# Performance work log

Hardware: AMD Instinct MI355X
Metric: run time of the kernel (lower is better)

Reference implementation:

```python
import jax, jax.numpy as jnp
import numpy as np

B, C, H, W = 4, 128, 128, 128
K = 9          # 3x3 kernel taps
TAU, BETA = 0.5, 10.0


def conv3x3(x, w, b):
    # x: (B,Cin,H,W), w: (Cout,Cin,3,3), stride 1, padding 1
    y = jax.lax.conv_general_dilated(
        x, w, window_strides=(1, 1), padding=((1, 1), (1, 1)),
        dimension_numbers=('NCHW', 'OIHW', 'NCHW'))
    return y + b[None, :, None, None]


def bilinear_sample(x, py, px):
    # x: (B,C,H,W); py,px: (B,K,H,W) fractional coords -> (B,C,K,H,W), zero outside
    Hi, Wi = x.shape[2], x.shape[3]
    y0 = jnp.floor(py); x0 = jnp.floor(px)
    y1 = y0 + 1.0;      x1 = x0 + 1.0
    ly = py - y0; lx = px - x0
    hy = 1.0 - ly; hx = 1.0 - lx
    xf = x.reshape(x.shape[0], x.shape[1], -1)  # (B,C,HW)

    def corner(yc, xc, wgt):
        valid = (yc >= 0) & (yc <= Hi - 1) & (xc >= 0) & (xc <= Wi - 1)
        yi = jnp.clip(yc, 0, Hi - 1).astype(jnp.int32)
        xi = jnp.clip(xc, 0, Wi - 1).astype(jnp.int32)
        idx = (yi * Wi + xi).reshape(yc.shape[0], -1)  # (B, K*H*W)
        g = jax.vmap(lambda f, i: f[:, i])(xf, idx)    # (B,C,K*H*W)
        g = g.reshape(x.shape[0], x.shape[1], *yc.shape[1:])  # (B,C,K,H,W)
        return g * (wgt * valid.astype(wgt.dtype))[:, None]

    return (corner(y0, x0, hy * hx) + corner(y0, x1, hy * lx)
            + corner(y1, x0, ly * hx) + corner(y1, x1, ly * lx))


def modulated_dcn(x, offset, mask, w, b):
    # offset: (B,2K,H,W) layout (dy,dx) per tap; mask: (B,K,H,W)
    Bn, Cn, Hn, Wn = x.shape
    off = offset.reshape(Bn, K, 2, Hn, Wn)
    dy, dx = off[:, :, 0], off[:, :, 1]
    ky, kx = jnp.meshgrid(jnp.arange(3), jnp.arange(3), indexing='ij')
    base_y = (ky.reshape(-1) - 1).astype(x.dtype)  # dilation=1, padding=1, stride=1
    base_x = (kx.reshape(-1) - 1).astype(x.dtype)
    hh = jnp.arange(Hn, dtype=x.dtype)
    ww = jnp.arange(Wn, dtype=x.dtype)
    py = hh[None, None, :, None] + base_y[None, :, None, None] + dy  # (B,K,H,W)
    px = ww[None, None, None, :] + base_x[None, :, None, None] + dx
    samp = bilinear_sample(x, py, px) * mask[:, None]  # (B,C,K,H,W)
    out = jnp.einsum('bckhw,ock->bohw', samp, w.reshape(w.shape[0], w.shape[1], K))
    return out + b[None, :, None, None]


def setup_inputs() -> dict:
    key = jax.random.key(0)
    ks = jax.random.split(key, 8)
    x = jax.random.normal(ks[0], (B, C, H, W), dtype=jnp.float32)
    U = jax.random.uniform(ks[1], (B, 1, H, W), dtype=jnp.float32)
    # conv_offset_mask: (3*K, C+1, 3, 3); small scale -> offsets of O(1) pixel
    w_om = jax.random.normal(ks[2], (3 * K, C + 1, 3, 3), dtype=jnp.float32) * 0.01
    b_om = jnp.zeros((3 * K,), dtype=jnp.float32)
    kaiming = float(np.sqrt(2.0 / (C * 9)))
    w_dcn = jax.random.normal(ks[3], (C, C, 3, 3), dtype=jnp.float32) * kaiming
    b_dcn = jnp.zeros((C,), dtype=jnp.float32)
    w1 = jax.random.normal(ks[4], (C, C, 3, 3), dtype=jnp.float32) * kaiming
    b1 = jnp.zeros((C,), dtype=jnp.float32)
    w2 = jax.random.normal(ks[5], (C, C, 3, 3), dtype=jnp.float32) * float(np.sqrt(1.0 / (C * 9)))
    b2 = jnp.zeros((C,), dtype=jnp.float32)
    return {"x": x, "U": U, "w_om": w_om, "b_om": b_om, "w_dcn": w_dcn,
            "b_dcn": b_dcn, "w1": w1, "b1": b1, "w2": w2, "b2": b2}


def reference(x, U, w_om, b_om, w_dcn, b_dcn, w1, b1, w2, b2):
    U = jnp.clip(U, 0.0, 1.0)
    guide = jnp.concatenate([x, U], axis=1)                # (B,C+1,H,W)
    om = conv3x3(guide, w_om, b_om)                        # (B,3K,H,W)
    offset = om[:, :2 * K]
    mask = 2.0 * jax.nn.sigmoid(om[:, 2 * K:])
    z = modulated_dcn(x, offset, mask, w_dcn, b_dcn)
    r = jax.nn.relu(conv3x3(z, w1, b1))
    r = conv3x3(r, w2, b2)
    gate = jax.nn.sigmoid(BETA * (U - TAU))
    return jax.nn.relu(x + r * gate)
```

## Files before the change

kernel.cpp:

```cpp
#include <hip/hip_runtime.h>
#include <math.h>

typedef unsigned int uint;
typedef unsigned short ushort;
typedef __attribute__((ext_vector_type(8))) __bf16 bf16x8;
typedef __attribute__((ext_vector_type(4))) float f32x4;

#define HW 16384

__device__ __forceinline__ ushort f2bf(float f) {
    uint u = __float_as_uint(f);
    u += 0x7fffu + ((u >> 16) & 1u);
    return (ushort)(u >> 16);
}
__device__ __forceinline__ void bhmap(int& b, int& h) {
    int lin = blockIdx.y * (int)gridDim.x + blockIdx.x;
    int n = (lin & 7) * 64 + (lin >> 3);
    h = n & 127;
    b = n >> 7;
}
__device__ __forceinline__ void bhmap2(int& b, int& h, int& px0) {
    int lin = blockIdx.x;
    int n = ((lin & 7) << 7) | (lin >> 3);
    b = n >> 8;
    int rm = n & 255;
    h = rm >> 1;
    px0 = (rm & 1) << 6;
}
__device__ __forceinline__ int swz(int row, int chunk) {
    return row * 128 + ((chunk ^ (row & 15)) << 3);
}
__device__ __forceinline__ uint blend2(uint a, uint b, uint c, uint d,
                                       float w00, float w01, float w10, float w11) {
    float lo = w00 * __uint_as_float(a << 16) + w01 * __uint_as_float(b << 16)
             + w10 * __uint_as_float(c << 16) + w11 * __uint_as_float(d << 16);
    float hi = w00 * __uint_as_float(a & 0xffff0000u) + w01 * __uint_as_float(b & 0xffff0000u)
             + w10 * __uint_as_float(c & 0xffff0000u) + w11 * __uint_as_float(d & 0xffff0000u);
    uint ul = __float_as_uint(lo); ul += 0x7fffu + ((ul >> 16) & 1u);
    uint uh = __float_as_uint(hi); uh += 0x7fffu + ((uh >> 16) & 1u);
    return (ul >> 16) | ((uh >> 16) << 16);
}

__global__ __launch_bounds__(256) void prep_w(
    const float* __restrict__ wd, const float* __restrict__ w1,
    const float* __restrict__ w2, const float* __restrict__ wom,
    ushort* __restrict__ wdt, ushort* __restrict__ w1B,
    ushort* __restrict__ w2B, ushort* __restrict__ womB,
    float* __restrict__ womu)
{
    int i = blockIdx.x * 256 + threadIdx.x;
    if (i < 147456) {
        int k = i >> 14, oc = (i >> 7) & 127, ci = i & 127;
        int s = (oc * 128 + ci) * 9 + k;
        wdt[i] = f2bf(wd[s]);
        int chunk = ci >> 3, kk = chunk >> 2, quad = chunk & 3, e = ci & 7;
        int d = ((((k * 8 + (oc >> 4)) * 4 + kk) * 4 + quad) * 16 + (oc & 15)) * 8 + e;
        w1B[d] = f2bf(w1[s]);
        w2B[d] = f2bf(w2[s]);
    }
    if (i < 36864) {
        int k = i >> 12, oc = (i >> 7) & 31, ci = i & 127;
        int chunk = ci >> 3, kk = chunk >> 2, quad = chunk & 3, e = ci & 7;
        int d = ((((k * 2 + (oc >> 4)) * 4 + kk) * 4 + quad) * 16 + (oc & 15)) * 8 + e;
        womB[d] = (oc < 27) ? f2bf(wom[(oc * 129 + ci) * 9 + k]) : (ushort)0;
    }
    if (i < 288) {
        int k = i >> 5, oc = i & 31;
        womu[i] = (oc < 27) ? wom[(oc * 129 + 128) * 9 + k] : 0.f;
    }
}

__global__ __launch_bounds__(256) void prep_xt(
    const float* __restrict__ x, ushort* __restrict__ xt)
{
    int b, h; bhmap(b, h);
    const int tid = threadIdx.x;
    __shared__ __align__(16) ushort T[128 * 136];
    const int w0 = tid & 127, cg = tid >> 7;
#pragma unroll 4
    for (int it = 0; it < 64; it++) {
        int c = it * 2 + cg;
        float f = x[((size_t)(b * 128 + c)) * HW + h * 128 + w0];
        T[w0 * 136 + c] = f2bf(f);
    }
    __syncthreads();
    const int w1 = tid >> 1, half = tid & 1;
    uint4* dst = (uint4*)(xt + (((size_t)b * HW) + h * 128 + w1) * 128 + half * 64);
    const uint4* src = (const uint4*)&T[w1 * 136 + half * 64];
#pragma unroll
    for (int c8 = 0; c8 < 8; c8++) dst[c8] = src[c8];
}

__device__ __forceinline__ void stage_halo(
    ushort* Hs, const ushort* __restrict__ src, int b, int h, int px0, int tid, int nthr)
{
    for (int s = tid; s < 396; s += nthr) {
        int r = s >> 1, half = s & 1;
        int ky = r / 66, xi = r - ky * 66;
        int gy = h - 1 + ky, gx = px0 - 1 + xi;
        if ((unsigned)gy < 128u && (unsigned)gx < 128u) {
            const uint4* p = (const uint4*)(src + (((size_t)b * HW) + gy * 128 + gx) * 128 + half * 64);
#pragma unroll
            for (int c = 0; c < 8; c++) *(uint4*)&Hs[swz(r, half * 8 + c)] = p[c];
        } else {
            uint4 zz = {0, 0, 0, 0};
#pragma unroll
            for (int c = 0; c < 8; c++) *(uint4*)&Hs[swz(r, half * 8 + c)] = zz;
        }
    }
}

__global__ __launch_bounds__(256, 3) void k_om(
    const ushort* __restrict__ xt, const float* __restrict__ U,
    const ushort* __restrict__ womB, const float* __restrict__ womu,
    const float* __restrict__ bom, float* __restrict__ omt)
{
    int b, h, px0; bhmap2(b, h, px0);
    const int tid = threadIdx.x;
    const int wid = tid >> 6, lane = tid & 63, lq = lane & 15, quad = lane >> 4;

    __shared__ __align__(16) ushort Hs[198 * 128];
    __shared__ float U3[3 * 66];
    __shared__ float wu[288];

    stage_halo(Hs, xt, b, h, px0, tid, 256);
    for (int s = tid; s < 198; s += 256) {
        int ky = s / 66, xi = s - ky * 66;
        int gy = h - 1 + ky, gx = px0 - 1 + xi;
        float v = 0.f;
        if ((unsigned)gy < 128u && (unsigned)gx < 128u) {
            v = U[(size_t)b * HW + gy * 128 + gx];
            v = fminf(fmaxf(v, 0.f), 1.f);
        }
        U3[s] = v;
    }
    for (int s = tid; s < 288; s += 256) wu[s] = womu[s];

    f32x4 acc[2];
#pragma unroll
    for (int j = 0; j < 2; j++)
#pragma unroll
        for (int r = 0; r < 4; r++) acc[j][r] = 0.f;

    bf16x8 bcur[2][4], bnext[2][4];
#pragma unroll
    for (int j = 0; j < 2; j++)
#pragma unroll
        for (int kk = 0; kk < 4; kk++)
            bcur[j][kk] = *(const bf16x8*)(womB + (size_t)((j * 4 + kk) * 512) + lane * 8);

    __syncthreads();

#pragma unroll
    for (int t9 = 0; t9 < 9; t9++) {
        if (t9 < 8) {
#pragma unroll
            for (int j = 0; j < 2; j++)
#pragma unroll
                for (int kk = 0; kk < 4; kk++)
                    bnext[j][kk] = *(const bf16x8*)(womB + (size_t)((((t9 + 1) * 2 + j) * 4 + kk) * 512) + lane * 8);
        }
        const int base = (t9 / 3) * 66 + (t9 % 3) + wid * 16;
#pragma unroll
        for (int kk = 0; kk < 4; kk++) {
            int chunk = kk * 4 + quad;
            bf16x8 av = *(const bf16x8*)&Hs[swz(base + lq, chunk)];
#pragma unroll
            for (int j = 0; j < 2; j++)
                acc[j] = __builtin_amdgcn_mfma_f32_16x16x32_bf16(av, bcur[j][kk], acc[j], 0, 0, 0);
        }
#pragma unroll
        for (int j = 0; j < 2; j++)
#pragma unroll
            for (int kk = 0; kk < 4; kk++) bcur[j][kk] = bnext[j][kk];
    }

#pragma unroll
    for (int j = 0; j < 2; j++) {
        int oc = j * 16 + lq;
        if (oc < 27) {
            float bias = bom[oc];
#pragma unroll
            for (int r = 0; r < 4; r++) {
                int pix = wid * 16 + quad * 4 + r;
                float v = acc[j][r] + bias;
#pragma unroll
                for (int t = 0; t < 9; t++)
                    v += U3[(t / 3) * 66 + pix + (t % 3)] * wu[t * 32 + oc];
                if (oc >= 18) v = 2.f / (1.f + __expf(-v));
                omt[((size_t)b * HW + h * 128 + px0 + pix) * 32 + oc] = v;
            }
        }
    }
}

__global__ __launch_bounds__(512, 4) void k_dcn(
    const ushort* __restrict__ xt, const float* __restrict__ omt,
    const ushort* __restrict__ wdt, const float* __restrict__ bdcn,
    ushort* __restrict__ zt)
{
    int b, h; bhmap(b, h);
    const int tid = threadIdx.x;
    const int wid = tid >> 6, lane = tid & 63, lq = lane & 15, quad = lane >> 4;
    const int pixbase = (wid & 1) * 64, ocbase = (wid >> 1) * 32;

    __shared__ __align__(16) ushort As[128 * 128];
    __shared__ __align__(16) ushort Bs[128 * 128];
    __shared__ __align__(16) int tbl[2][128][8];

    const int sc = lane & 15;
    const int sp = lane >> 4;

    f32x4 acc[4][2];
#pragma unroll
    for (int i = 0; i < 4; i++)
#pragma unroll
        for (int j = 0; j < 2; j++)
#pragma unroll
            for (int r = 0; r < 4; r++) acc[i][j][r] = 0.f;

    const float* omrow = omt + ((size_t)b * HW + h * 128) * 32;
    const ushort* xtb = xt + (size_t)b * HW * 128;

    auto build = [&](int k, int buf) {
        if (tid < 128) {
            int p = tid;
            float dyv = omrow[p * 32 + 2 * k];
            float dxv = omrow[p * 32 + 2 * k + 1];
            float m   = omrow[p * 32 + 18 + k];
            float fy = (float)(h + k / 3 - 1) + dyv;
            float fx = (float)(p + k % 3 - 1) + dxv;
            float y0f = floorf(fy), x0f = floorf(fx);
            float ly = fy - y0f, lx = fx - x0f;
            float hy = 1.f - ly, hx = 1.f - lx;
            bool vy0 = (y0f >= 0.f) && (y0f <= 127.f);
            bool vy1 = (y0f >= -1.f) && (y0f <= 126.f);
            bool vx0 = (x0f >= 0.f) && (x0f <= 127.f);
            bool vx1 = (x0f >= -1.f) && (x0f <= 126.f);
            float w00 = (vy0 && vx0) ? hy * hx * m : 0.f;
            float w01 = (vy0 && vx1) ? hy * lx * m : 0.f;
            float w10 = (vy1 && vx0) ? ly * hx * m : 0.f;
            float w11 = (vy1 && vx1) ? ly * lx * m : 0.f;
            int iy0 = min(max((int)y0f, 0), 127);
            int iy1 = min(max((int)y0f + 1, 0), 127);
            int ix0 = min(max((int)x0f, 0), 127);
            int ix1 = min(max((int)x0f + 1, 0), 127);
            int* tp = &tbl[buf][p][0];
            tp[0] = (iy0 * 128 + ix0) * 128;
            tp[1] = (iy0 * 128 + ix1) * 128;
            tp[2] = (iy1 * 128 + ix0) * 128;
            tp[3] = (iy1 * 128 + ix1) * 128;
            ((float*)tp)[4] = w00; ((float*)tp)[5] = w01;
            ((float*)tp)[6] = w10; ((float*)tp)[7] = w11;
        }
    };

    build(0, 0);
    __syncthreads();

    const int brow = tid >> 2, bq = tid & 3;
    for (int k = 0; k < 9; k++) {
        const int buf = k & 1;
        {
            const uint4* src = (const uint4*)(wdt + (size_t)k * 16384 + brow * 128 + bq * 32);
#pragma unroll
            for (int c = 0; c < 4; c++) *(uint4*)&Bs[swz(brow, bq * 4 + c)] = src[c];
        }
        const ushort* basep = xtb + sc * 8;
#pragma unroll 2
        for (int r = 0; r < 4; r++) {
            int p = r * 32 + wid * 4 + sp;
            int4 off = *(const int4*)&tbl[buf][p][0];
            f32x4 wv = *(const f32x4*)((const float*)&tbl[buf][p][0] + 4);
            uint4 q00 = *(const uint4*)(basep + off.x);
            uint4 q01 = *(const uint4*)(basep + off.y);
            uint4 q10 = *(const uint4*)(basep + off.z);
            uint4 q11 = *(const uint4*)(basep + off.w);
            uint4 st;
            st.x = blend2(q00.x, q01.x, q10.x, q11.x, wv[0], wv[1], wv[2], wv[3]);
            st.y = blend2(q00.y, q01.y, q10.y, q11.y, wv[0], wv[1], wv[2], wv[3]);
            st.z = blend2(q00.z, q01.z, q10.z, q11.z, wv[0], wv[1], wv[2], wv[3]);
            st.w = blend2(q00.w, q01.w, q10.w, q11.w, wv[0], wv[1], wv[2], wv[3]);
            *(uint4*)&As[swz(p, sc)] = st;
        }
        __syncthreads();
        if (k < 8) build(k + 1, buf ^ 1);
#pragma unroll
        for (int kk = 0; kk < 4; kk++) {
            int chunk = kk * 4 + quad;
            bf16x8 av[4], bv[2];
#pragma unroll
            for (int j = 0; j < 2; j++) bv[j] = *(const bf16x8*)&Bs[swz(ocbase + j * 16 + lq, chunk)];
#pragma unroll
            for (int i = 0; i < 4; i++) av[i] = *(const bf16x8*)&As[swz(pixbase + i * 16 + lq, chunk)];
#pragma unroll
            for (int i = 0; i < 4; i++)
#pragma unroll
                for (int j = 0; j < 2; j++)
                    acc[i][j] = __builtin_amdgcn_mfma_f32_16x16x32_bf16(av[i], bv[j], acc[i][j], 0, 0, 0);
        }
        __syncthreads();
    }

    size_t prow = ((size_t)b * HW + h * 128) * 128;
#pragma unroll
    for (int j = 0; j < 2; j++) {
        int oc = ocbase + j * 16 + lq;
        float bias = bdcn[oc];
#pragma unroll
        for (int i = 0; i < 4; i++)
#pragma unroll
            for (int r = 0; r < 4; r++) {
                int pix = pixbase + i * 16 + quad * 4 + r;
                zt[prow + (size_t)pix * 128 + oc] = f2bf(acc[i][j][r] + bias);
            }
    }
}

__global__ __launch_bounds__(256, 3) void k_conv1(
    const ushort* __restrict__ zt, const ushort* __restrict__ w1B,
    const float* __restrict__ b1, ushort* __restrict__ r1t)
{
    int b, h, px0; bhmap2(b, h, px0);
    const int tid = threadIdx.x;
    const int wid = tid >> 6, lane = tid & 63, lq = lane & 15, quad = lane >> 4;
    const int ocbase = wid * 32, ocg = wid * 2;

    __shared__ __align__(16) ushort Hs[198 * 128];

    stage_halo(Hs, zt, b, h, px0, tid, 256);

    f32x4 acc[4][2];
#pragma unroll
    for (int i = 0; i < 4; i++)
#pragma unroll
        for (int j = 0; j < 2; j++)
#pragma unroll
            for (int r = 0; r < 4; r++) acc[i][j][r] = 0.f;

    bf16x8 bcur[2][4], bnext[2][4];
#pragma unroll
    for (int j = 0; j < 2; j++)
#pragma unroll
        for (int kk = 0; kk < 4; kk++)
            bcur[j][kk] = *(const bf16x8*)(w1B + (size_t)(((ocg + j) * 4 + kk) * 512) + lane * 8);

    __syncthreads();

#pragma unroll
    for (int t9 = 0; t9 < 9; t9++) {
        if (t9 < 8) {
#pragma unroll
            for (int j = 0; j < 2; j++)
#pragma unroll
                for (int kk = 0; kk < 4; kk++)
                    bnext[j][kk] = *(const bf16x8*)(w1B + (size_t)((((t9 + 1) * 8 + ocg + j) * 4 + kk) * 512) + lane * 8);
        }
        const int base = (t9 / 3) * 66 + (t9 % 3);
#pragma unroll
        for (int kk = 0; kk < 4; kk++) {
            int chunk = kk * 4 + quad;
            bf16x8 av[4];
#pragma unroll
            for (int i = 0; i < 4; i++)
                av[i] = *(const bf16x8*)&Hs[swz(base + i * 16 + lq, chunk)];
#pragma unroll
            for (int i = 0; i < 4; i++)
#pragma unroll
                for (int j = 0; j < 2; j++)
                    acc[i][j] = __builtin_amdgcn_mfma_f32_16x16x32_bf16(av[i], bcur[j][kk], acc[i][j], 0, 0, 0);
        }
#pragma unroll
        for (int j = 0; j < 2; j++)
#pragma unroll
            for (int kk = 0; kk < 4; kk++) bcur[j][kk] = bnext[j][kk];
    }

    size_t prow = ((size_t)b * HW + h * 128 + px0) * 128;
#pragma unroll
    for (int j = 0; j < 2; j++) {
        int oc = ocbase + j * 16 + lq;
        float bias = b1[oc];
#pragma unroll
        for (int i = 0; i < 4; i++)
#pragma unroll
            for (int r = 0; r < 4; r++) {
                int pix = i * 16 + quad * 4 + r;
                r1t[prow + (size_t)pix * 128 + oc] = f2bf(fmaxf(acc[i][j][r] + bias, 0.f));
            }
    }
}

__global__ __launch_bounds__(256, 3) void k_conv2(
    const ushort* __restrict__ r1t, const ushort* __restrict__ w2B,
    const float* __restrict__ b2, const float* __restrict__ x,
    const float* __restrict__ U, float* __restrict__ out)
{
    int b, h, px0; bhmap2(b, h, px0);
    const int tid = threadIdx.x;
    const int wid = tid >> 6, lane = tid & 63, lq = lane & 15, quad = lane >> 4;
    const int ocbase = wid * 32, ocg = wid * 2;

    __shared__ __align__(16) ushort Hs[198 * 128];

    stage_halo(Hs, r1t, b, h, px0, tid, 256);

    f32x4 acc[2][4];
#pragma unroll
    for (int i = 0; i < 2; i++)
#pragma unroll
        for (int j = 0; j < 4; j++)
#pragma unroll
            for (int r = 0; r < 4; r++) acc[i][j][r] = 0.f;

    bf16x8 acur[2][4], anext[2][4];
#pragma unroll
    for (int i = 0; i < 2; i++)
#pragma unroll
        for (int kk = 0; kk < 4; kk++)
            acur[i][kk] = *(const bf16x8*)(w2B + (size_t)(((ocg + i) * 4 + kk) * 512) + lane * 8);

    __syncthreads();

#pragma unroll
    for (int t9 = 0; t9 < 9; t9++) {
        if (t9 < 8) {
#pragma unroll
            for (int i = 0; i < 2; i++)
#pragma unroll
                for (int kk = 0; kk < 4; kk++)
                    anext[i][kk] = *(const bf16x8*)(w2B + (size_t)((((t9 + 1) * 8 + ocg + i) * 4 + kk) * 512) + lane * 8);
        }
        const int base = (t9 / 3) * 66 + (t9 % 3);
#pragma unroll
        for (int kk = 0; kk < 4; kk++) {
            int chunk = kk * 4 + quad;
            bf16x8 bv[4];
#pragma unroll
            for (int j = 0; j < 4; j++)
                bv[j] = *(const bf16x8*)&Hs[swz(base + j * 16 + lq, chunk)];
#pragma unroll
            for (int i = 0; i < 2; i++)
#pragma unroll
                for (int j = 0; j < 4; j++)
                    acc[i][j] = __builtin_amdgcn_mfma_f32_16x16x32_bf16(acur[i][kk], bv[j], acc[i][j], 0, 0, 0);
        }
#pragma unroll
        for (int i = 0; i < 2; i++)
#pragma unroll
            for (int kk = 0; kk < 4; kk++) acur[i][kk] = anext[i][kk];
    }

#pragma unroll
    for (int j = 0; j < 4; j++) {
        int pix = j * 16 + lq;
        float u = U[(size_t)b * HW + h * 128 + px0 + pix];
        u = fminf(fmaxf(u, 0.f), 1.f);
        float g = 1.f / (1.f + __expf(-10.f * (u - 0.5f)));
#pragma unroll
        for (int i = 0; i < 2; i++) {
            f32x4 b4 = *(const f32x4*)&b2[ocbase + i * 16 + quad * 4];
#pragma unroll
            for (int r = 0; r < 4; r++) {
                int oc = ocbase + i * 16 + quad * 4 + r;
                size_t idx = ((size_t)(b * 128 + oc)) * HW + h * 128 + px0 + pix;
                float v = acc[i][j][r] + b4[r];
                out[idx] = fmaxf(x[idx] + v * g, 0.f);
            }
        }
    }
}

extern "C" void kernel_launch(void* const* d_in, const int* in_sizes, int n_in,
                              void* d_out, int out_size, void* d_ws, size_t ws_size,
                              hipStream_t stream)
{
    const float* x     = (const float*)d_in[0];
    const float* U     = (const float*)d_in[1];
    const float* w_om  = (const float*)d_in[2];
    const float* b_om  = (const float*)d_in[3];
    const float* w_dcn = (const float*)d_in[4];
    const float* b_dcn = (const float*)d_in[5];
    const float* w1    = (const float*)d_in[6];
    const float* b1    = (const float*)d_in[7];
    const float* w2    = (const float*)d_in[8];
    const float* b2    = (const float*)d_in[9];
    float* out = (float*)d_out;

    char* p = (char*)d_ws;
    ushort* xt   = (ushort*)p; p += (size_t)4 * HW * 128 * 2;
    ushort* zt   = (ushort*)p; p += (size_t)4 * HW * 128 * 2;
    ushort* r1t  = (ushort*)p; p += (size_t)4 * HW * 128 * 2;
    float*  omt  = (float*)p;  p += (size_t)4 * HW * 32 * 4;
    ushort* wdt  = (ushort*)p; p += 147456 * 2;
    ushort* w1B  = (ushort*)p; p += 147456 * 2;
    ushort* w2B  = (ushort*)p; p += 147456 * 2;
    ushort* womB = (ushort*)p; p += 36864 * 2;
    float*  womu = (float*)p;  p += 288 * 4;

    prep_w<<<576, 256, 0, stream>>>(w_dcn, w1, w2, w_om, wdt, w1B, w2B, womB, womu);
    prep_xt<<<dim3(128, 4), 256, 0, stream>>>(x, xt);
    k_om<<<1024, 256, 0, stream>>>(xt, U, womB, womu, b_om, omt);
    k_dcn<<<dim3(128, 4), 512, 0, stream>>>(xt, omt, wdt, b_dcn, zt);
    k_conv1<<<1024, 256, 0, stream>>>(zt, w1B, b1, r1t);
    k_conv2<<<1024, 256, 0, stream>>>(r1t, w2B, b2, x, U, out);
}
```

Before: 239.6 us.

## Fuse offset/mask conv into DCN kernel and stream DCN weights from registers

```diff
diff --git a/kernel.cpp b/kernel.cpp
--- a/kernel.cpp
+++ b/kernel.cpp
@@ -44,7 +44,7 @@
 __global__ __launch_bounds__(256) void prep_w(
     const float* __restrict__ wd, const float* __restrict__ w1,
     const float* __restrict__ w2, const float* __restrict__ wom,
-    ushort* __restrict__ wdt, ushort* __restrict__ w1B,
+    ushort* __restrict__ wdB, ushort* __restrict__ w1B,
     ushort* __restrict__ w2B, ushort* __restrict__ womB,
     float* __restrict__ womu)
 {
@@ -52,9 +52,9 @@
     if (i < 147456) {
         int k = i >> 14, oc = (i >> 7) & 127, ci = i & 127;
         int s = (oc * 128 + ci) * 9 + k;
-        wdt[i] = f2bf(wd[s]);
         int chunk = ci >> 3, kk = chunk >> 2, quad = chunk & 3, e = ci & 7;
         int d = ((((k * 8 + (oc >> 4)) * 4 + kk) * 4 + quad) * 16 + (oc & 15)) * 8 + e;
+        wdB[d] = f2bf(wd[s]);
         w1B[d] = f2bf(w1[s]);
         w2B[d] = f2bf(w2[s]);
     }
@@ -110,23 +110,27 @@
     }
 }
 
-__global__ __launch_bounds__(256, 3) void k_om(
+__global__ __launch_bounds__(512, 4) void k_dcn(
     const ushort* __restrict__ xt, const float* __restrict__ U,
     const ushort* __restrict__ womB, const float* __restrict__ womu,
-    const float* __restrict__ bom, float* __restrict__ omt)
-{
-    int b, h, px0; bhmap2(b, h, px0);
+    const float* __restrict__ bom,
+    const ushort* __restrict__ wdB, const float* __restrict__ bdcn,
+    ushort* __restrict__ zt)
+{
+    int b, h; bhmap(b, h);
     const int tid = threadIdx.x;
     const int wid = tid >> 6, lane = tid & 63, lq = lane & 15, quad = lane >> 4;
 
-    __shared__ __align__(16) ushort Hs[198 * 128];
-    __shared__ float U3[3 * 66];
+    __shared__ __align__(16) ushort As[128 * 128];
+    __shared__ float omL[128][33];
+    __shared__ __align__(16) int tbl[2][128][8];
+    __shared__ float U3[3 * 130];
     __shared__ float wu[288];
 
-    stage_halo(Hs, xt, b, h, px0, tid, 256);
-    for (int s = tid; s < 198; s += 256) {
-        int ky = s / 66, xi = s - ky * 66;
-        int gy = h - 1 + ky, gx = px0 - 1 + xi;
+    const ushort* xtb = xt + (size_t)b * HW * 128;
+
+    for (int s = tid; s < 390; s += 512) {
+        int r = s / 130, c = s % 130, gy = h - 1 + r, gx = c - 1;
         float v = 0.f;
         if ((unsigned)gy < 128u && (unsigned)gx < 128u) {
             v = U[(size_t)b * HW + gy * 128 + gx];
@@ -134,47 +138,56 @@
         }
         U3[s] = v;
     }
-    for (int s = tid; s < 288; s += 256) wu[s] = womu[s];
-
-    f32x4 acc[2];
+    if (tid < 288) wu[tid] = womu[tid];
+
+    f32x4 aco[2];
 #pragma unroll
     for (int j = 0; j < 2; j++)
 #pragma unroll
-        for (int r = 0; r < 4; r++) acc[j][r] = 0.f;
-
-    bf16x8 bcur[2][4], bnext[2][4];
+        for (int r = 0; r < 4; r++) aco[j][r] = 0.f;
+
+    bf16x8 bocur[2][4], bonext[2][4];
 #pragma unroll
     for (int j = 0; j < 2; j++)
 #pragma unroll
         for (int kk = 0; kk < 4; kk++)
-            bcur[j][kk] = *(const bf16x8*)(womB + (size_t)((j * 4 + kk) * 512) + lane * 8);
-
-    __syncthreads();
-
+            bocur[j][kk] = *(const bf16x8*)(womB + (size_t)((j * 4 + kk) * 512) + lane * 8);
+
+    const int arow = tid >> 2, aq = tid & 3;
 #pragma unroll
     for (int t9 = 0; t9 < 9; t9++) {
+        int gy = h + t9 / 3 - 1, gx = arow + t9 % 3 - 1;
+        if ((unsigned)gy < 128u && (unsigned)gx < 128u) {
+            const uint4* src = (const uint4*)(xtb + ((size_t)(gy * 128 + gx)) * 128 + aq * 32);
+#pragma unroll
+            for (int c = 0; c < 4; c++) *(uint4*)&As[swz(arow, aq * 4 + c)] = src[c];
+        } else {
+            uint4 zz = {0, 0, 0, 0};
+#pragma unroll
+            for (int c = 0; c < 4; c++) *(uint4*)&As[swz(arow, aq * 4 + c)] = zz;
+        }
+        __syncthreads();
         if (t9 < 8) {
 #pragma unroll
             for (int j = 0; j < 2; j++)
 #pragma unroll
                 for (int kk = 0; kk < 4; kk++)
-                    bnext[j][kk] = *(const bf16x8*)(womB + (size_t)((((t9 + 1) * 2 + j) * 4 + kk) * 512) + lane * 8);
-        }
-        const int base = (t9 / 3) * 66 + (t9 % 3) + wid * 16;
+                    bonext[j][kk] = *(const bf16x8*)(womB + (size_t)((((t9 + 1) * 2 + j) * 4 + kk) * 512) + lane * 8);
+        }
 #pragma unroll
         for (int kk = 0; kk < 4; kk++) {
             int chunk = kk * 4 + quad;
-            bf16x8 av = *(const bf16x8*)&Hs[swz(base + lq, chunk)];
+            bf16x8 av = *(const bf16x8*)&As[swz(wid * 16 + lq, chunk)];
 #pragma unroll
             for (int j = 0; j < 2; j++)
-                acc[j] = __builtin_amdgcn_mfma_f32_16x16x32_bf16(av, bcur[j][kk], acc[j], 0, 0, 0);
+                aco[j] = __builtin_amdgcn_mfma_f32_16x16x32_bf16(av, bocur[j][kk], aco[j], 0, 0, 0);
         }
 #pragma unroll
         for (int j = 0; j < 2; j++)
 #pragma unroll
-            for (int kk = 0; kk < 4; kk++) bcur[j][kk] = bnext[j][kk];
-    }
-
+            for (int kk = 0; kk < 4; kk++) bocur[j][kk] = bonext[j][kk];
+        __syncthreads();
+    }
 #pragma unroll
     for (int j = 0; j < 2; j++) {
         int oc = j * 16 + lq;
@@ -183,31 +196,18 @@
 #pragma unroll
             for (int r = 0; r < 4; r++) {
                 int pix = wid * 16 + quad * 4 + r;
-                float v = acc[j][r] + bias;
+                float v = aco[j][r] + bias;
 #pragma unroll
                 for (int t = 0; t < 9; t++)
-                    v += U3[(t / 3) * 66 + pix + (t % 3)] * wu[t * 32 + oc];
+                    v += U3[(t / 3) * 130 + pix + (t % 3)] * wu[t * 32 + oc];
                 if (oc >= 18) v = 2.f / (1.f + __expf(-v));
-                omt[((size_t)b * HW + h * 128 + px0 + pix) * 32 + oc] = v;
+                omL[pix][oc] = v;
             }
         }
     }
-}
-
-__global__ __launch_bounds__(512, 4) void k_dcn(
-    const ushort* __restrict__ xt, const float* __restrict__ omt,
-    const ushort* __restrict__ wdt, const float* __restrict__ bdcn,
-    ushort* __restrict__ zt)
-{
-    int b, h; bhmap(b, h);
-    const int tid = threadIdx.x;
-    const int wid = tid >> 6, lane = tid & 63, lq = lane & 15, quad = lane >> 4;
-    const int pixbase = (wid & 1) * 64, ocbase = (wid >> 1) * 32;
-
-    __shared__ __align__(16) ushort As[128 * 128];
-    __shared__ __align__(16) ushort Bs[128 * 128];
-    __shared__ __align__(16) int tbl[2][128][8];
-
+    __syncthreads();
+
+    const int pixbase = (wid & 1) * 64, ocbase = (wid >> 1) * 32, ocg = (wid >> 1) * 2;
     const int sc = lane & 15;
     const int sp = lane >> 4;
 
@@ -218,16 +218,13 @@
         for (int j = 0; j < 2; j++)
 #pragma unroll
             for (int r = 0; r < 4; r++) acc[i][j][r] = 0.f;
-
-    const float* omrow = omt + ((size_t)b * HW + h * 128) * 32;
-    const ushort* xtb = xt + (size_t)b * HW * 128;
 
     auto build = [&](int k, int buf) {
         if (tid < 128) {
             int p = tid;
-            float dyv = omrow[p * 32 + 2 * k];
-            float dxv = omrow[p * 32 + 2 * k + 1];
-            float m   = omrow[p * 32 + 18 + k];
+            float dyv = omL[p][2 * k];
+            float dxv = omL[p][2 * k + 1];
+            float m   = omL[p][18 + k];
             float fy = (float)(h + k / 3 - 1) + dyv;
             float fx = (float)(p + k % 3 - 1) + dxv;
             float y0f = floorf(fy), x0f = floorf(fx);
@@ -256,16 +253,18 @@
     };
 
     build(0, 0);
+
+    bf16x8 bdcur[2][4], bdnext[2][4];
+#pragma unroll
+    for (int j = 0; j < 2; j++)
+#pragma unroll
+        for (int kk = 0; kk < 4; kk++)
+            bdcur[j][kk] = *(const bf16x8*)(wdB + (size_t)(((ocg + j) * 4 + kk) * 512) + lane * 8);
+
     __syncthreads();
 
-    const int brow = tid >> 2, bq = tid & 3;
     for (int k = 0; k < 9; k++) {
         const int buf = k & 1;
-        {
-            const uint4* src = (const uint4*)(wdt + (size_t)k * 16384 + brow * 128 + bq * 32);
-#pragma unroll
-            for (int c = 0; c < 4; c++) *(uint4*)&Bs[swz(brow, bq * 4 + c)] = src[c];
-        }
         const ushort* basep = xtb + sc * 8;
 #pragma unroll 2
         for (int r = 0; r < 4; r++) {
@@ -284,21 +283,30 @@
             *(uint4*)&As[swz(p, sc)] = st;
         }
         __syncthreads();
-        if (k < 8) build(k + 1, buf ^ 1);
+        if (k < 8) {
+            build(k + 1, buf ^ 1);
+#pragma unroll
+            for (int j = 0; j < 2; j++)
+#pragma unroll
+                for (int kk = 0; kk < 4; kk++)
+                    bdnext[j][kk] = *(const bf16x8*)(wdB + (size_t)((((k + 1) * 8 + ocg + j) * 4 + kk) * 512) + lane * 8);
+        }
 #pragma unroll
         for (int kk = 0; kk < 4; kk++) {
             int chunk = kk * 4 + quad;
-            bf16x8 av[4], bv[2];
-#pragma unroll
-            for (int j = 0; j < 2; j++) bv[j] = *(const bf16x8*)&Bs[swz(ocbase + j * 16 + lq, chunk)];
+            bf16x8 av[4];
 #pragma unroll
             for (int i = 0; i < 4; i++) av[i] = *(const bf16x8*)&As[swz(pixbase + i * 16 + lq, chunk)];
 #pragma unroll
             for (int i = 0; i < 4; i++)
 #pragma unroll
                 for (int j = 0; j < 2; j++)
-                    acc[i][j] = __builtin_amdgcn_mfma_f32_16x16x32_bf16(av[i], bv[j], acc[i][j], 0, 0, 0);
-        }
+                    acc[i][j] = __builtin_amdgcn_mfma_f32_16x16x32_bf16(av[i], bdcur[j][kk], acc[i][j], 0, 0, 0);
+        }
+#pragma unroll
+        for (int j = 0; j < 2; j++)
+#pragma unroll
+            for (int kk = 0; kk < 4; kk++) bdcur[j][kk] = bdnext[j][kk];
         __syncthreads();
     }
 
@@ -491,17 +499,15 @@
     ushort* xt   = (ushort*)p; p += (size_t)4 * HW * 128 * 2;
     ushort* zt   = (ushort*)p; p += (size_t)4 * HW * 128 * 2;
     ushort* r1t  = (ushort*)p; p += (size_t)4 * HW * 128 * 2;
-    float*  omt  = (float*)p;  p += (size_t)4 * HW * 32 * 4;
-    ushort* wdt  = (ushort*)p; p += 147456 * 2;
+    ushort* wdB  = (ushort*)p; p += 147456 * 2;
     ushort* w1B  = (ushort*)p; p += 147456 * 2;
     ushort* w2B  = (ushort*)p; p += 147456 * 2;
     ushort* womB = (ushort*)p; p += 36864 * 2;
     float*  womu = (float*)p;  p += 288 * 4;
 
-    prep_w<<<576, 256, 0, stream>>>(w_dcn, w1, w2, w_om, wdt, w1B, w2B, womB, womu);
+    prep_w<<<576, 256, 0, stream>>>(w_dcn, w1, w2, w_om, wdB, w1B, w2B, womB, womu);
     prep_xt<<<dim3(128, 4), 256, 0, stream>>>(x, xt);
-    k_om<<<1024, 256, 0, stream>>>(xt, U, womB, womu, b_om, omt);
-    k_dcn<<<dim3(128, 4), 512, 0, stream>>>(xt, omt, wdt, b_dcn, zt);
+    k_dcn<<<dim3(128, 4), 512, 0, stream>>>(xt, U, womB, womu, b_om, wdB, b_dcn, zt);
     k_conv1<<<1024, 256, 0, stream>>>(zt, w1B, b1, r1t);
     k_conv2<<<1024, 256, 0, stream>>>(r1t, w2B, b2, x, U, out);
 }
```

New measurement: 257.9 us. 7.6% more time.
